# Kernel optimization log

Measured on AMD Instinct MI355X. Metric: run time of the kernel, lower is better.

## Reference

```python
import jax, jax.numpy as jnp
import numpy as np

N_GRAPHS = 256

def gcn_conv(x, src, dst, W, b, n_nodes):
    # PyG GCNConv: add self-loops, symmetric normalization, then aggregate x_j*norm at dst.
    loop = jnp.arange(n_nodes, dtype=src.dtype)
    row = jnp.concatenate([src, loop])
    col = jnp.concatenate([dst, loop])
    h = x @ W  # [N, out]
    deg = jax.ops.segment_sum(jnp.ones_like(col, dtype=h.dtype), col, num_segments=n_nodes)
    dinv = jnp.where(deg > 0, jax.lax.rsqrt(deg), 0.0)
    norm = dinv[row] * dinv[col]  # [E+N]
    msg = h[row] * norm[:, None]
    out = jax.ops.segment_sum(msg, col, num_segments=n_nodes)
    return out + b

def global_mean_pool(x, batch, num_graphs):
    s = jax.ops.segment_sum(x, batch, num_segments=num_graphs)
    cnt = jax.ops.segment_sum(jnp.ones((x.shape[0],), dtype=x.dtype), batch, num_segments=num_graphs)
    return s / jnp.maximum(cnt, 1.0)[:, None]

def setup_inputs() -> dict:
    key = jax.random.key(0)
    ks = jax.random.split(key, 9)
    N, E, F, H = 100000, 3200000, 136, 50
    x = jax.random.normal(ks[0], (N, F), dtype=jnp.float32)
    edge_index = jax.random.randint(ks[1], (2, E), 0, N, dtype=jnp.int64)
    batch = jnp.sort(jax.random.randint(ks[2], (N,), 0, N_GRAPHS, dtype=jnp.int64))
    s1 = 1.0 / np.sqrt(F)
    s2 = 1.0 / np.sqrt(H)
    W1 = jax.random.uniform(ks[3], (F, H), jnp.float32, -s1, s1)
    b1 = jnp.zeros((H,), jnp.float32)
    W2 = jax.random.uniform(ks[4], (H, H), jnp.float32, -s2, s2)
    b2 = jnp.zeros((H,), jnp.float32)
    Wl = jax.random.uniform(ks[5], (H, 1), jnp.float32, -s2, s2)
    bl = jnp.zeros((1,), jnp.float32)
    return {"x": x, "edge_index": edge_index, "batch": batch,
            "W1": W1, "b1": b1, "W2": W2, "b2": b2, "Wl": Wl, "bl": bl}

def reference(x, edge_index, batch, W1, b1, W2, b2, Wl, bl):
    n = x.shape[0]
    src, dst = edge_index[0], edge_index[1]
    h = jax.nn.relu(gcn_conv(x, src, dst, W1, b1, n))
    h = jax.nn.relu(gcn_conv(h, src, dst, W2, b2, n))
    g = global_mean_pool(h, batch, N_GRAPHS)
    # Dropout is inference-identity (deterministic baseline).
    out = jax.nn.sigmoid(g @ Wl + bl)
    return out.flatten()
```

## Files before the change

### kernel.cpp

```cpp
#include <hip/hip_runtime.h>
#include <math.h>

#define HH 50
#define BSH 8
#define BSZ 256
#define CH 8192
#define SCH 4096

typedef float floatx2 __attribute__((ext_vector_type(2)));

__device__ __forceinline__ unsigned int f2bf_pair(float f0, float f1) {
    unsigned int u0 = __float_as_uint(f0);
    unsigned int u1 = __float_as_uint(f1);
    u0 = (u0 + 0x7FFFu + ((u0 >> 16) & 1u)) >> 16;
    u1 = (u1 + 0x7FFFu + ((u1 >> 16) & 1u)) >> 16;
    return u0 | (u1 << 16);
}
__device__ __forceinline__ float bf_lo(unsigned int p) { return __uint_as_float(p << 16); }
__device__ __forceinline__ float bf_hi(unsigned int p) { return __uint_as_float(p & 0xFFFF0000u); }

__device__ __forceinline__ unsigned int pack4_fp8(float f0, float f1, float f2, float f3) {
    int r = 0;
    r = __builtin_amdgcn_cvt_pk_fp8_f32(f0, f1, r, false);
    r = __builtin_amdgcn_cvt_pk_fp8_f32(f2, f3, r, true);
    return (unsigned int)r;
}

__global__ void histA_kernel(const int* __restrict__ ei, int E, int NB, int NC,
                             int* __restrict__ blockHist) {
    __shared__ int hist[512];
    int c = blockIdx.x;
    int tid = threadIdx.x;
    for (int i = tid; i < 512; i += 256) hist[i] = 0;
    __syncthreads();
    int beg = c * CH, end = min(E, beg + CH);
    for (int i = beg + tid; i < end; i += 256) {
        int d = ei[(size_t)E + i];
        atomicAdd(&hist[d >> BSH], 1);
    }
    __syncthreads();
    for (int i = tid; i < NB; i += 256) blockHist[i * NC + c] = hist[i];
}

__global__ void scan1_kernel(const int* __restrict__ bh, int M, int* __restrict__ csum) {
    __shared__ int red[4];
    int tid = threadIdx.x;
    int lane = tid & 63, wv = tid >> 6;
    int base = blockIdx.x * SCH + tid * 16;
    int s = 0;
    if (base + 16 <= M) {
#pragma unroll
        for (int j = 0; j < 4; j++) {
            int4 v = *(const int4*)(bh + base + 4 * j);
            s += v.x + v.y + v.z + v.w;
        }
    } else {
        for (int j = 0; j < 16 && base + j < M; j++) s += bh[base + j];
    }
    for (int off = 1; off < 64; off <<= 1) s += __shfl_xor(s, off);
    if (lane == 0) red[wv] = s;
    __syncthreads();
    if (tid == 0) csum[blockIdx.x] = red[0] + red[1] + red[2] + red[3];
}

__global__ void scan2_kernel(int* __restrict__ csum, int nb,
                             int* __restrict__ rowptr, int N, int E) {
    int lane = threadIdx.x;
    int v = (lane < nb) ? csum[lane] : 0;
    int orig = v;
    for (int off = 1; off < 64; off <<= 1) {
        int u = __shfl_up(v, off);
        if (lane >= off) v += u;
    }
    if (lane < nb) csum[lane] = v - orig;
    if (lane == 0) rowptr[N] = E;
}

__global__ void scan3_kernel(const int* __restrict__ bh, int M, const int* __restrict__ csum,
                             int* __restrict__ scanned) {
    __shared__ int wsum[4];
    int tid = threadIdx.x;
    int lane = tid & 63, wv = tid >> 6;
    int base = blockIdx.x * SCH + tid * 16;
    int a[16];
#pragma unroll
    for (int j = 0; j < 16; j++) a[j] = 0;
    if (base + 16 <= M) {
#pragma unroll
        for (int j = 0; j < 4; j++) {
            int4 v = *(const int4*)(bh + base + 4 * j);
            a[4 * j] = v.x; a[4 * j + 1] = v.y; a[4 * j + 2] = v.z; a[4 * j + 3] = v.w;
        }
    } else {
        for (int j = 0; j < 16 && base + j < M; j++) a[j] = bh[base + j];
    }
    int t = 0;
#pragma unroll
    for (int j = 0; j < 16; j++) t += a[j];
    int inc = t;
    for (int off = 1; off < 64; off <<= 1) {
        int u = __shfl_up(inc, off);
        if (lane >= off) inc += u;
    }
    if (lane == 63) wsum[wv] = inc;
    __syncthreads();
    int wb = 0;
    for (int w = 0; w < wv; w++) wb += wsum[w];
    int run = csum[blockIdx.x] + wb + (inc - t);
    if (base + 16 <= M) {
#pragma unroll
        for (int j = 0; j < 4; j++) {
            int4 o;
            o.x = run; run += a[4 * j];
            o.y = run; run += a[4 * j + 1];
            o.z = run; run += a[4 * j + 2];
            o.w = run; run += a[4 * j + 3];
            *(int4*)(scanned + base + 4 * j) = o;
        }
    } else {
        for (int j = 0; j < 16 && base + j < M; j++) { scanned[base + j] = run; run += a[j]; }
    }
}

__global__ void scatterB_kernel(const int* __restrict__ ei, int E, int NB, int NC,
                                const int* __restrict__ blockHist,
                                const int* __restrict__ scanned, int* __restrict__ ebuf) {
    __shared__ int part[512];
    __shared__ int lofs[512];
    __shared__ int gofs[512];
    __shared__ int cur[512];
    __shared__ int epack[CH];
    int c = blockIdx.x;
    int tid = threadIdx.x;
    int v = (tid < NB) ? blockHist[tid * NC + c] : 0;
    part[tid] = v;
    __syncthreads();
    for (int off = 1; off < 512; off <<= 1) {
        int u = (tid >= off) ? part[tid - off] : 0;
        __syncthreads();
        part[tid] += u;
        __syncthreads();
    }
    int ex = (tid == 0) ? 0 : part[tid - 1];
    lofs[tid] = ex;
    cur[tid] = ex;
    if (tid < NB) gofs[tid] = scanned[tid * NC + c];
    __syncthreads();
    int beg = c * CH, end = min(E, beg + CH), len = end - beg;
    for (int i = beg + tid; i < end; i += 512) {
        int s = ei[i];
        int d = ei[(size_t)E + i];
        int b = d >> BSH;
        int pos = atomicAdd(&cur[b], 1);
        epack[pos] = ((d & (BSZ - 1)) << 17) | s;
    }
    __syncthreads();
    for (int j = tid; j < len; j += 512) {
        int lo = 0, hi = NB - 1;
        while (lo < hi) { int mid = (lo + hi + 1) >> 1; if (lofs[mid] <= j) lo = mid; else hi = mid - 1; }
        ebuf[gofs[lo] + (j - lofs[lo])] = epack[j];
    }
}

__global__ void buildC_kernel(const int* __restrict__ ebuf, const int* __restrict__ scanned,
                              int NB, int NC, int N, int E,
                              int* __restrict__ rowptr, float* __restrict__ dinv,
                              int* __restrict__ colidx) {
    __shared__ int cnt[BSZ], woff[BSZ], part[BSZ];
    int b = blockIdx.x;
    int tid = threadIdx.x;
    int ebeg = scanned[b * NC];
    int eend = (b == NB - 1) ? E : scanned[(b + 1) * NC];
    if (tid < BSZ) cnt[tid] = 0;
    __syncthreads();
    for (int i = ebeg + tid; i < eend; i += 512) {
        atomicAdd(&cnt[ebuf[i] >> 17], 1);
    }
    __syncthreads();
    if (tid < BSZ) part[tid] = cnt[tid];
    __syncthreads();
    for (int off = 1; off < BSZ; off <<= 1) {
        int v = 0;
        if (tid < BSZ && tid >= off) v = part[tid - off];
        __syncthreads();
        if (tid < BSZ) part[tid] += v;
        __syncthreads();
    }
    if (tid < BSZ) {
        int ex = (tid == 0) ? 0 : part[tid - 1];
        woff[tid] = ex;
        int node = (b << BSH) + tid;
        if (node < N) {
            rowptr[node] = ebeg + ex;
            dinv[node] = 1.0f / sqrtf((float)(cnt[tid] + 1));
        }
    }
    __syncthreads();
    for (int i = ebeg + tid; i < eend; i += 512) {
        int p = ebuf[i];
        int dl = p >> 17;
        int s = p & 0x1FFFF;
        int pos = atomicAdd(&woff[dl], 1);
        colidx[ebeg + pos] = s;
    }
}

__global__ void gemm_f32_kernel(const float* __restrict__ in, int K, int f4stride,
                                const float* __restrict__ W, int H,
                                const float* __restrict__ dinv,
                                unsigned int* __restrict__ hsA,
                                unsigned int* __restrict__ hsB, int N) {
    __shared__ float xs[16][128];
    __shared__ float ws[16][64];
    int tid = threadIdx.x;
    int row0 = blockIdx.x * 128;
    int rg = tid >> 3;
    int cg = tid & 7;
    int rl = tid >> 1;
    int h  = tid & 1;
    float acc[4][8];
#pragma unroll
    for (int r = 0; r < 4; r++)
#pragma unroll
        for (int c = 0; c < 8; c++) acc[r][c] = 0.0f;
    const float4* inf4 = (const float4*)in;
    int rowA = row0 + rl;

    for (int k0 = 0; k0 < K; k0 += 16) {
        for (int i = tid; i < 1024; i += 256) {
            int k = i >> 6, c = i & 63;
            ws[k][c] = (k0 + k < K && c < H) ? W[(k0 + k) * H + c] : 0.0f;
        }
        {
            int qa = h, qb = h + 2;
            int g1 = min((k0 >> 2) + qa, f4stride - 1);
            int g2 = min((k0 >> 2) + qb, f4stride - 1);
            float4 xv1 = make_float4(0.f, 0.f, 0.f, 0.f), xv2 = xv1;
            if (rowA < N) {
                xv1 = inf4[(size_t)rowA * f4stride + g1];
                xv2 = inf4[(size_t)rowA * f4stride + g2];
            }
            xs[qa * 4 + 0][rl] = xv1.x; xs[qa * 4 + 1][rl] = xv1.y;
            xs[qa * 4 + 2][rl] = xv1.z; xs[qa * 4 + 3][rl] = xv1.w;
            xs[qb * 4 + 0][rl] = xv2.x; xs[qb * 4 + 1][rl] = xv2.y;
            xs[qb * 4 + 2][rl] = xv2.z; xs[qb * 4 + 3][rl] = xv2.w;
        }
        __syncthreads();
#pragma unroll
        for (int k = 0; k < 16; k++) {
            float4 xa = *(const float4*)&xs[k][rg * 4];
            float4 wa = *(const float4*)&ws[k][cg * 8];
            float4 wb = *(const float4*)&ws[k][cg * 8 + 4];
            float xr[4] = {xa.x, xa.y, xa.z, xa.w};
            float wc[8] = {wa.x, wa.y, wa.z, wa.w, wb.x, wb.y, wb.z, wb.w};
#pragma unroll
            for (int r = 0; r < 4; r++)
#pragma unroll
                for (int c = 0; c < 8; c++) acc[r][c] += xr[r] * wc[c];
        }
        __syncthreads();
    }
#pragma unroll
    for (int r = 0; r < 4; r++) {
        int row = row0 + rg * 4 + r;
        if (row < N) {
            float dv = dinv[row];
            uint2 o;
            o.x = pack4_fp8(acc[r][0] * dv, acc[r][1] * dv, acc[r][2] * dv, acc[r][3] * dv);
            o.y = pack4_fp8(acc[r][4] * dv, acc[r][5] * dv, acc[r][6] * dv, acc[r][7] * dv);
            if (cg < 4) ((uint2*)(hsA + (size_t)row * 8))[cg] = o;
            else        ((uint2*)(hsB + (size_t)row * 8))[cg - 4] = o;
        }
    }
}

__global__ void gemm_bf16_kernel(const unsigned int* __restrict__ in, int K,
                                 const float* __restrict__ W, int H,
                                 const float* __restrict__ dinv,
                                 unsigned int* __restrict__ hsA,
                                 unsigned int* __restrict__ hsB, int N) {
    __shared__ float xs[16][128];
    __shared__ float ws[16][64];
    int tid = threadIdx.x;
    int row0 = blockIdx.x * 128;
    int rg = tid >> 3;
    int cg = tid & 7;
    int rl = tid >> 1;
    int h  = tid & 1;
    float acc[4][8];
#pragma unroll
    for (int r = 0; r < 4; r++)
#pragma unroll
        for (int c = 0; c < 8; c++) acc[r][c] = 0.0f;
    const uint2* inu2 = (const uint2*)in;
    int rowA = row0 + rl;
    int KP = 64;

    for (int k0 = 0; k0 < KP; k0 += 16) {
        for (int i = tid; i < 1024; i += 256) {
            int k = i >> 6, c = i & 63;
            ws[k][c] = (k0 + k < K && c < H) ? W[(k0 + k) * H + c] : 0.0f;
        }
        {
            int qa = h, qb = h + 2;
            int g1 = (k0 >> 2) + qa;
            int g2 = (k0 >> 2) + qb;
            uint2 xv1 = make_uint2(0u, 0u), xv2 = xv1;
            if (rowA < N) {
                xv1 = inu2[(size_t)rowA * 16 + g1];
                xv2 = inu2[(size_t)rowA * 16 + g2];
            }
            xs[qa * 4 + 0][rl] = bf_lo(xv1.x); xs[qa * 4 + 1][rl] = bf_hi(xv1.x);
            xs[qa * 4 + 2][rl] = bf_lo(xv1.y); xs[qa * 4 + 3][rl] = bf_hi(xv1.y);
            xs[qb * 4 + 0][rl] = bf_lo(xv2.x); xs[qb * 4 + 1][rl] = bf_hi(xv2.x);
            xs[qb * 4 + 2][rl] = bf_lo(xv2.y); xs[qb * 4 + 3][rl] = bf_hi(xv2.y);
        }
        __syncthreads();
#pragma unroll
        for (int k = 0; k < 16; k++) {
            float4 xa = *(const float4*)&xs[k][rg * 4];
            float4 wa = *(const float4*)&ws[k][cg * 8];
            float4 wb = *(const float4*)&ws[k][cg * 8 + 4];
            float xr[4] = {xa.x, xa.y, xa.z, xa.w};
            float wc[8] = {wa.x, wa.y, wa.z, wa.w, wb.x, wb.y, wb.z, wb.w};
#pragma unroll
            for (int r = 0; r < 4; r++)
#pragma unroll
                for (int c = 0; c < 8; c++) acc[r][c] += xr[r] * wc[c];
        }
        __syncthreads();
    }
#pragma unroll
    for (int r = 0; r < 4; r++) {
        int row = row0 + rg * 4 + r;
        if (row < N) {
            float dv = dinv[row];
            uint2 o;
            o.x = pack4_fp8(acc[r][0] * dv, acc[r][1] * dv, acc[r][2] * dv, acc[r][3] * dv);
            o.y = pack4_fp8(acc[r][4] * dv, acc[r][5] * dv, acc[r][6] * dv, acc[r][7] * dv);
            if (cg < 4) ((uint2*)(hsA + (size_t)row * 8))[cg] = o;
            else        ((uint2*)(hsB + (size_t)row * 8))[cg - 4] = o;
        }
    }
}

__global__ void agg_half_kernel(const unsigned int* __restrict__ hsh,
                                const int* __restrict__ rowptr, const int* __restrict__ colidx,
                                const float* __restrict__ dinv, const float* __restrict__ bias,
                                int cbase, unsigned int* __restrict__ outbuf, int N) {
    int t = blockIdx.x * blockDim.x + threadIdx.x;
    int node = t >> 3;
    int q = t & 7;
    if (node >= N) return;
    const unsigned int* basq = hsh + q;
    unsigned int sv = basq[(size_t)node * 8];
    floatx2 plo = __builtin_amdgcn_cvt_pk_f32_fp8((int)sv, false);
    floatx2 phi = __builtin_amdgcn_cvt_pk_f32_fp8((int)sv, true);
    float a0 = plo[0], a1 = plo[1], a2 = phi[0], a3 = phi[1];
    int beg = rowptr[node], end = rowptr[node + 1];
    int e = beg;
    for (; e + 4 <= end; e += 4) {
        int s0 = colidx[e], s1 = colidx[e + 1], s2 = colidx[e + 2], s3 = colidx[e + 3];
        unsigned int v0 = basq[(size_t)s0 * 8];
        unsigned int v1 = basq[(size_t)s1 * 8];
        unsigned int v2 = basq[(size_t)s2 * 8];
        unsigned int v3 = basq[(size_t)s3 * 8];
        floatx2 l0 = __builtin_amdgcn_cvt_pk_f32_fp8((int)v0, false);
        floatx2 h0 = __builtin_amdgcn_cvt_pk_f32_fp8((int)v0, true);
        floatx2 l1 = __builtin_amdgcn_cvt_pk_f32_fp8((int)v1, false);
        floatx2 h1 = __builtin_amdgcn_cvt_pk_f32_fp8((int)v1, true);
        floatx2 l2 = __builtin_amdgcn_cvt_pk_f32_fp8((int)v2, false);
        floatx2 h2 = __builtin_amdgcn_cvt_pk_f32_fp8((int)v2, true);
        floatx2 l3 = __builtin_amdgcn_cvt_pk_f32_fp8((int)v3, false);
        floatx2 h3 = __builtin_amdgcn_cvt_pk_f32_fp8((int)v3, true);
        a0 += (l0[0] + l1[0]) + (l2[0] + l3[0]);
        a1 += (l0[1] + l1[1]) + (l2[1] + l3[1]);
        a2 += (h0[0] + h1[0]) + (h2[0] + h3[0]);
        a3 += (h0[1] + h1[1]) + (h2[1] + h3[1]);
    }
    for (; e < end; e++) {
        int s0 = colidx[e];
        unsigned int v0 = basq[(size_t)s0 * 8];
        floatx2 l0 = __builtin_amdgcn_cvt_pk_f32_fp8((int)v0, false);
        floatx2 h0 = __builtin_amdgcn_cvt_pk_f32_fp8((int)v0, true);
        a0 += l0[0]; a1 += l0[1]; a2 += h0[0]; a3 += h0[1];
    }
    float dv = dinv[node];
    int c0 = cbase + q * 4;
    float b0 = (c0 + 0 < HH) ? bias[c0 + 0] : 0.0f;
    float b1 = (c0 + 1 < HH) ? bias[c0 + 1] : 0.0f;
    float b2 = (c0 + 2 < HH) ? bias[c0 + 2] : 0.0f;
    float b3 = (c0 + 3 < HH) ? bias[c0 + 3] : 0.0f;
    float r0 = fmaxf(a0 * dv + b0, 0.0f);
    float r1 = fmaxf(a1 * dv + b1, 0.0f);
    float r2 = fmaxf(a2 * dv + b2, 0.0f);
    float r3 = fmaxf(a3 * dv + b3, 0.0f);
    uint2 w;
    if (c0 >= HH) { w.x = 0u; w.y = 0u; }
    else { w.x = f2bf_pair(r0, r1); w.y = f2bf_pair(r2, r3); }
    ((uint2*)outbuf)[(size_t)node * 16 + (cbase >> 2) + q] = w;
}

__global__ void pool_head_kernel(const unsigned int* __restrict__ h,
                                 const int* __restrict__ batch, int N,
                                 const float* __restrict__ Wl, const float* __restrict__ bl,
                                 float* __restrict__ out, int G) {
    __shared__ float4 red[16][16];
    int b = blockIdx.x;
    int t = threadIdx.x;
    int sub = t >> 4, q = t & 15;
    int beg, end;
    {
        int lo = 0, hi = N;
        while (lo < hi) { int mid = (lo + hi) >> 1; if (batch[mid] < b) lo = mid + 1; else hi = mid; }
        beg = lo;
        lo = 0; hi = N;
        while (lo < hi) { int mid = (lo + hi) >> 1; if (batch[mid] < b + 1) lo = mid + 1; else hi = mid; }
        end = lo;
    }
    const uint2* base = (const uint2*)h;
    float4 acc = make_float4(0.f, 0.f, 0.f, 0.f);
    for (int node = beg + sub; node < end; node += 16) {
        uint2 v = base[(size_t)node * 16 + q];
        acc.x += bf_lo(v.x); acc.y += bf_hi(v.x); acc.z += bf_lo(v.y); acc.w += bf_hi(v.y);
    }
    red[sub][q] = acc;
    __syncthreads();
#pragma unroll
    for (int off = 8; off >= 1; off >>= 1) {
        if (sub < off) {
            float4 a = red[sub][q], c = red[sub + off][q];
            a.x += c.x; a.y += c.y; a.z += c.z; a.w += c.w;
            red[sub][q] = a;
        }
        __syncthreads();
    }
    if (t == 0) {
        const float* g = (const float*)&red[0][0];
        float dot = 0.0f;
        for (int c = 0; c < HH; c++) dot += g[c] * Wl[c];
        float cnt = (float)(end - beg);
        float x = dot / fmaxf(cnt, 1.0f) + bl[0];
        out[b] = 1.0f / (1.0f + expf(-x));
    }
}

extern "C" void kernel_launch(void* const* d_in, const int* in_sizes, int n_in,
                              void* d_out, int out_size, void* d_ws, size_t ws_size,
                              hipStream_t stream) {
    const float* x     = (const float*)d_in[0];
    const int*   ei    = (const int*)d_in[1];
    const int*   batch = (const int*)d_in[2];
    const float* W1    = (const float*)d_in[3];
    const float* b1    = (const float*)d_in[4];
    const float* W2    = (const float*)d_in[5];
    const float* b2    = (const float*)d_in[6];
    const float* Wl    = (const float*)d_in[7];
    const float* bl    = (const float*)d_in[8];
    float* out = (float*)d_out;

    int N = in_sizes[2];
    int E = in_sizes[1] / 2;
    int F = in_sizes[0] / N;
    int G = out_size;

    int NB = (N + BSZ - 1) >> BSH;
    int NC = (E + CH - 1) / CH;
    int M  = NB * NC;
    int NS = (M + SCH - 1) / SCH;

    char* ws = (char*)d_ws;
    size_t off = 0;
    auto alloc = [&](size_t bytes) -> void* {
        void* p = ws + off;
        off += (bytes + 255) & ~(size_t)255;
        return p;
    };
    size_t halfBytes = (size_t)N * 32;
    size_t bufBytes  = (size_t)N * 128;
    size_t ebufBytes = (size_t)E * 4;
    float*        dinv      = (float*)alloc((size_t)N * 4);
    int*          rowptr    = (int*)alloc((size_t)(N + 1) * 4);
    int*          colidx    = (int*)alloc(ebufBytes);
    unsigned int* hsA       = (unsigned int*)alloc(halfBytes);
    unsigned int* hsB       = (unsigned int*)alloc(halfBytes);
    unsigned int* buf       = (unsigned int*)alloc(bufBytes > ebufBytes ? bufBytes : ebufBytes);
    int*          blockHist = (int*)alloc((size_t)M * 4);
    int*          scanned   = (int*)alloc((size_t)M * 4);
    int*          csum      = (int*)alloc((size_t)NS * 4 + 256);
    int*          ebuf      = (int*)buf;

    histA_kernel<<<NC, 256, 0, stream>>>(ei, E, NB, NC, blockHist);
    scan1_kernel<<<NS, 256, 0, stream>>>(blockHist, M, csum);
    scan2_kernel<<<1, 64, 0, stream>>>(csum, NS, rowptr, N, E);
    scan3_kernel<<<NS, 256, 0, stream>>>(blockHist, M, csum, scanned);
    scatterB_kernel<<<NC, 512, 0, stream>>>(ei, E, NB, NC, blockHist, scanned, ebuf);
    buildC_kernel<<<NB, 512, 0, stream>>>(ebuf, scanned, NB, NC, N, E, rowptr, dinv, colidx);

    int aggBlocks = ((N * 8) + 255) / 256;
    int gemmBlocks = (N + 127) / 128;

    gemm_f32_kernel<<<gemmBlocks, 256, 0, stream>>>(x, F, F / 4, W1, HH, dinv, hsA, hsB, N);
    agg_half_kernel<<<aggBlocks, 256, 0, stream>>>(hsA, rowptr, colidx, dinv, b1, 0,  buf, N);
    agg_half_kernel<<<aggBlocks, 256, 0, stream>>>(hsB, rowptr, colidx, dinv, b1, 32, buf, N);

    gemm_bf16_kernel<<<gemmBlocks, 256, 0, stream>>>(buf, 50, W2, HH, dinv, hsA, hsB, N);
    agg_half_kernel<<<aggBlocks, 256, 0, stream>>>(hsA, rowptr, colidx, dinv, b2, 0,  buf, N);
    agg_half_kernel<<<aggBlocks, 256, 0, stream>>>(hsB, rowptr, colidx, dinv, b2, 32, buf, N);

    pool_head_kernel<<<G, 256, 0, stream>>>(buf, batch, N, Wl, bl, out, G);
}
```

Measured before the change: 257.7 us.

## Replace FP32 SIMT GEMMs with bf16 MFMA 16x16x32 kernels

Both dense transforms (x@W1 and h@W2) are rewritten to use bf16 MFMA instructions. Each wave handles 16 rows, the weights are staged transposed in bf16 in LDS, and results go through an LDS tile so the epilogue can scale by dinv and pack to fp8. This targets the FP32 FMA cost and shared-memory traffic of the old tiled GEMMs, at the price of rounding x and W1 to bf16, which adds precision loss. The GEMMs are a small part of a pipeline dominated by aggregation, so the overall effect is bounded.

```diff
diff --git a/kernel.cpp b/kernel.cpp
--- a/kernel.cpp
+++ b/kernel.cpp
@@ -8,6 +8,10 @@
 #define SCH 4096
 
 typedef float floatx2 __attribute__((ext_vector_type(2)));
+typedef float f32x4 __attribute__((ext_vector_type(4)));
+typedef short short8v __attribute__((ext_vector_type(8)));
+
+union ABfrag { short8v s; unsigned int u[4]; };
 
 __device__ __forceinline__ unsigned int f2bf_pair(float f0, float f1) {
     unsigned int u0 = __float_as_uint(f0);
@@ -205,142 +209,130 @@
     }
 }
 
-__global__ void gemm_f32_kernel(const float* __restrict__ in, int K, int f4stride,
-                                const float* __restrict__ W, int H,
-                                const float* __restrict__ dinv,
-                                unsigned int* __restrict__ hsA,
-                                unsigned int* __restrict__ hsB, int N) {
-    __shared__ float xs[16][128];
-    __shared__ float ws[16][64];
-    int tid = threadIdx.x;
-    int row0 = blockIdx.x * 128;
-    int rg = tid >> 3;
-    int cg = tid & 7;
-    int rl = tid >> 1;
-    int h  = tid & 1;
-    float acc[4][8];
-#pragma unroll
-    for (int r = 0; r < 4; r++)
-#pragma unroll
-        for (int c = 0; c < 8; c++) acc[r][c] = 0.0f;
-    const float4* inf4 = (const float4*)in;
-    int rowA = row0 + rl;
-
-    for (int k0 = 0; k0 < K; k0 += 16) {
-        for (int i = tid; i < 1024; i += 256) {
-            int k = i >> 6, c = i & 63;
-            ws[k][c] = (k0 + k < K && c < H) ? W[(k0 + k) * H + c] : 0.0f;
-        }
-        {
-            int qa = h, qb = h + 2;
-            int g1 = min((k0 >> 2) + qa, f4stride - 1);
-            int g2 = min((k0 >> 2) + qb, f4stride - 1);
-            float4 xv1 = make_float4(0.f, 0.f, 0.f, 0.f), xv2 = xv1;
-            if (rowA < N) {
-                xv1 = inf4[(size_t)rowA * f4stride + g1];
-                xv2 = inf4[(size_t)rowA * f4stride + g2];
-            }
-            xs[qa * 4 + 0][rl] = xv1.x; xs[qa * 4 + 1][rl] = xv1.y;
-            xs[qa * 4 + 2][rl] = xv1.z; xs[qa * 4 + 3][rl] = xv1.w;
-            xs[qb * 4 + 0][rl] = xv2.x; xs[qb * 4 + 1][rl] = xv2.y;
-            xs[qb * 4 + 2][rl] = xv2.z; xs[qb * 4 + 3][rl] = xv2.w;
-        }
-        __syncthreads();
-#pragma unroll
-        for (int k = 0; k < 16; k++) {
-            float4 xa = *(const float4*)&xs[k][rg * 4];
-            float4 wa = *(const float4*)&ws[k][cg * 8];
-            float4 wb = *(const float4*)&ws[k][cg * 8 + 4];
-            float xr[4] = {xa.x, xa.y, xa.z, xa.w};
-            float wc[8] = {wa.x, wa.y, wa.z, wa.w, wb.x, wb.y, wb.z, wb.w};
-#pragma unroll
-            for (int r = 0; r < 4; r++)
-#pragma unroll
-                for (int c = 0; c < 8; c++) acc[r][c] += xr[r] * wc[c];
-        }
-        __syncthreads();
-    }
+__global__ void gemm1_mfma(const float* __restrict__ x, int K, int H,
+                           const float* __restrict__ W,
+                           const float* __restrict__ dinv,
+                           unsigned int* __restrict__ hsA,
+                           unsigned int* __restrict__ hsB, int N) {
+    const int KP = 160, S = 168;
+    __shared__ unsigned short wsT[64 * S];
+    __shared__ float ls[4][16][64];
+    int tid = threadIdx.x;
+    int w = tid >> 6, lane = tid & 63;
+    int row0 = blockIdx.x * 64 + w * 16;
+    for (int i = tid; i < KP * 64; i += 256) {
+        int k = i >> 6, col = i & 63;
+        float v = (k < K && col < H) ? W[k * H + col] : 0.0f;
+        wsT[col * S + k] = (unsigned short)(f2bf_pair(v, 0.0f) & 0xFFFFu);
+    }
+    __syncthreads();
+
+    int arow = row0 + (lane & 15);
+    int kgrp = (lane >> 4) * 8;
+    f32x4 acc0 = 0.0f, acc1 = 0.0f, acc2 = 0.0f, acc3 = 0.0f;
+    for (int k0 = 0; k0 < KP; k0 += 32) {
+        int koff = k0 + kgrp;
+        ABfrag a; a.u[0] = 0; a.u[1] = 0; a.u[2] = 0; a.u[3] = 0;
+        if (arow < N && koff < K) {
+            const float* xp = x + (size_t)arow * K + koff;
+            float4 v1 = *(const float4*)xp;
+            float4 v2 = *(const float4*)(xp + 4);
+            a.u[0] = f2bf_pair(v1.x, v1.y); a.u[1] = f2bf_pair(v1.z, v1.w);
+            a.u[2] = f2bf_pair(v2.x, v2.y); a.u[3] = f2bf_pair(v2.z, v2.w);
+        }
+        ABfrag b0, b1, b2, b3;
+        b0.s = *(const short8v*)&wsT[(0 * 16 + (lane & 15)) * S + koff];
+        b1.s = *(const short8v*)&wsT[(1 * 16 + (lane & 15)) * S + koff];
+        b2.s = *(const short8v*)&wsT[(2 * 16 + (lane & 15)) * S + koff];
+        b3.s = *(const short8v*)&wsT[(3 * 16 + (lane & 15)) * S + koff];
+        acc0 = __builtin_amdgcn_mfma_f32_16x16x32_bf16(a.s, b0.s, acc0, 0, 0, 0);
+        acc1 = __builtin_amdgcn_mfma_f32_16x16x32_bf16(a.s, b1.s, acc1, 0, 0, 0);
+        acc2 = __builtin_amdgcn_mfma_f32_16x16x32_bf16(a.s, b2.s, acc2, 0, 0, 0);
+        acc3 = __builtin_amdgcn_mfma_f32_16x16x32_bf16(a.s, b3.s, acc3, 0, 0, 0);
+    }
+    int r4 = (lane >> 4) * 4;
 #pragma unroll
     for (int r = 0; r < 4; r++) {
-        int row = row0 + rg * 4 + r;
-        if (row < N) {
-            float dv = dinv[row];
-            uint2 o;
-            o.x = pack4_fp8(acc[r][0] * dv, acc[r][1] * dv, acc[r][2] * dv, acc[r][3] * dv);
-            o.y = pack4_fp8(acc[r][4] * dv, acc[r][5] * dv, acc[r][6] * dv, acc[r][7] * dv);
-            if (cg < 4) ((uint2*)(hsA + (size_t)row * 8))[cg] = o;
-            else        ((uint2*)(hsB + (size_t)row * 8))[cg - 4] = o;
-        }
-    }
-}
-
-__global__ void gemm_bf16_kernel(const unsigned int* __restrict__ in, int K,
-                                 const float* __restrict__ W, int H,
-                                 const float* __restrict__ dinv,
-                                 unsigned int* __restrict__ hsA,
-                                 unsigned int* __restrict__ hsB, int N) {
-    __shared__ float xs[16][128];
-    __shared__ float ws[16][64];
-    int tid = threadIdx.x;
-    int row0 = blockIdx.x * 128;
-    int rg = tid >> 3;
-    int cg = tid & 7;
-    int rl = tid >> 1;
-    int h  = tid & 1;
-    float acc[4][8];
-#pragma unroll
-    for (int r = 0; r < 4; r++)
-#pragma unroll
-        for (int c = 0; c < 8; c++) acc[r][c] = 0.0f;
-    const uint2* inu2 = (const uint2*)in;
-    int rowA = row0 + rl;
-    int KP = 64;
-
-    for (int k0 = 0; k0 < KP; k0 += 16) {
-        for (int i = tid; i < 1024; i += 256) {
-            int k = i >> 6, c = i & 63;
-            ws[k][c] = (k0 + k < K && c < H) ? W[(k0 + k) * H + c] : 0.0f;
-        }
-        {
-            int qa = h, qb = h + 2;
-            int g1 = (k0 >> 2) + qa;
-            int g2 = (k0 >> 2) + qb;
-            uint2 xv1 = make_uint2(0u, 0u), xv2 = xv1;
-            if (rowA < N) {
-                xv1 = inu2[(size_t)rowA * 16 + g1];
-                xv2 = inu2[(size_t)rowA * 16 + g2];
-            }
-            xs[qa * 4 + 0][rl] = bf_lo(xv1.x); xs[qa * 4 + 1][rl] = bf_hi(xv1.x);
-            xs[qa * 4 + 2][rl] = bf_lo(xv1.y); xs[qa * 4 + 3][rl] = bf_hi(xv1.y);
-            xs[qb * 4 + 0][rl] = bf_lo(xv2.x); xs[qb * 4 + 1][rl] = bf_hi(xv2.x);
-            xs[qb * 4 + 2][rl] = bf_lo(xv2.y); xs[qb * 4 + 3][rl] = bf_hi(xv2.y);
-        }
-        __syncthreads();
-#pragma unroll
-        for (int k = 0; k < 16; k++) {
-            float4 xa = *(const float4*)&xs[k][rg * 4];
-            float4 wa = *(const float4*)&ws[k][cg * 8];
-            float4 wb = *(const float4*)&ws[k][cg * 8 + 4];
-            float xr[4] = {xa.x, xa.y, xa.z, xa.w};
-            float wc[8] = {wa.x, wa.y, wa.z, wa.w, wb.x, wb.y, wb.z, wb.w};
-#pragma unroll
-            for (int r = 0; r < 4; r++)
-#pragma unroll
-                for (int c = 0; c < 8; c++) acc[r][c] += xr[r] * wc[c];
-        }
-        __syncthreads();
-    }
+        ls[w][r4 + r][0 * 16 + (lane & 15)] = acc0[r];
+        ls[w][r4 + r][1 * 16 + (lane & 15)] = acc1[r];
+        ls[w][r4 + r][2 * 16 + (lane & 15)] = acc2[r];
+        ls[w][r4 + r][3 * 16 + (lane & 15)] = acc3[r];
+    }
+    __syncthreads();
+    int prow = lane >> 2, cg = lane & 3;
+    int row = row0 + prow;
+    if (row < N) {
+        float dv = dinv[row];
+        const float* lr = &ls[w][prow][cg * 16];
+        uint4 o;
+        o.x = pack4_fp8(lr[0] * dv, lr[1] * dv, lr[2] * dv, lr[3] * dv);
+        o.y = pack4_fp8(lr[4] * dv, lr[5] * dv, lr[6] * dv, lr[7] * dv);
+        o.z = pack4_fp8(lr[8] * dv, lr[9] * dv, lr[10] * dv, lr[11] * dv);
+        o.w = pack4_fp8(lr[12] * dv, lr[13] * dv, lr[14] * dv, lr[15] * dv);
+        if (cg < 2) ((uint4*)(hsA + (size_t)row * 8))[cg] = o;
+        else        ((uint4*)(hsB + (size_t)row * 8))[cg - 2] = o;
+    }
+}
+
+__global__ void gemm2_mfma(const unsigned int* __restrict__ in, int K, int H,
+                           const float* __restrict__ W,
+                           const float* __restrict__ dinv,
+                           unsigned int* __restrict__ hsA,
+                           unsigned int* __restrict__ hsB, int N) {
+    const int KP = 64, S = 72;
+    __shared__ unsigned short wsT[64 * S];
+    __shared__ float ls[4][16][64];
+    int tid = threadIdx.x;
+    int w = tid >> 6, lane = tid & 63;
+    int row0 = blockIdx.x * 64 + w * 16;
+    for (int i = tid; i < KP * 64; i += 256) {
+        int k = i >> 6, col = i & 63;
+        float v = (k < K && col < H) ? W[k * H + col] : 0.0f;
+        wsT[col * S + k] = (unsigned short)(f2bf_pair(v, 0.0f) & 0xFFFFu);
+    }
+    __syncthreads();
+
+    int arow = row0 + (lane & 15);
+    int kgrp = (lane >> 4) * 8;
+    f32x4 acc0 = 0.0f, acc1 = 0.0f, acc2 = 0.0f, acc3 = 0.0f;
+    for (int k0 = 0; k0 < KP; k0 += 32) {
+        int koff = k0 + kgrp;
+        ABfrag a; a.u[0] = 0; a.u[1] = 0; a.u[2] = 0; a.u[3] = 0;
+        if (arow < N) {
+            uint4 v = *(const uint4*)(in + (size_t)arow * 32 + (koff >> 1));
+            a.u[0] = v.x; a.u[1] = v.y; a.u[2] = v.z; a.u[3] = v.w;
+        }
+        ABfrag b0, b1, b2, b3;
+        b0.s = *(const short8v*)&wsT[(0 * 16 + (lane & 15)) * S + koff];
+        b1.s = *(const short8v*)&wsT[(1 * 16 + (lane & 15)) * S + koff];
+        b2.s = *(const short8v*)&wsT[(2 * 16 + (lane & 15)) * S + koff];
+        b3.s = *(const short8v*)&wsT[(3 * 16 + (lane & 15)) * S + koff];
+        acc0 = __builtin_amdgcn_mfma_f32_16x16x32_bf16(a.s, b0.s, acc0, 0, 0, 0);
+        acc1 = __builtin_amdgcn_mfma_f32_16x16x32_bf16(a.s, b1.s, acc1, 0, 0, 0);
+        acc2 = __builtin_amdgcn_mfma_f32_16x16x32_bf16(a.s, b2.s, acc2, 0, 0, 0);
+        acc3 = __builtin_amdgcn_mfma_f32_16x16x32_bf16(a.s, b3.s, acc3, 0, 0, 0);
+    }
+    int r4 = (lane >> 4) * 4;
 #pragma unroll
     for (int r = 0; r < 4; r++) {
-        int row = row0 + rg * 4 + r;
-        if (row < N) {
-            float dv = dinv[row];
-            uint2 o;
-            o.x = pack4_fp8(acc[r][0] * dv, acc[r][1] * dv, acc[r][2] * dv, acc[r][3] * dv);
-            o.y = pack4_fp8(acc[r][4] * dv, acc[r][5] * dv, acc[r][6] * dv, acc[r][7] * dv);
-            if (cg < 4) ((uint2*)(hsA + (size_t)row * 8))[cg] = o;
-            else        ((uint2*)(hsB + (size_t)row * 8))[cg - 4] = o;
-        }
+        ls[w][r4 + r][0 * 16 + (lane & 15)] = acc0[r];
+        ls[w][r4 + r][1 * 16 + (lane & 15)] = acc1[r];
+        ls[w][r4 + r][2 * 16 + (lane & 15)] = acc2[r];
+        ls[w][r4 + r][3 * 16 + (lane & 15)] = acc3[r];
+    }
+    __syncthreads();
+    int prow = lane >> 2, cg = lane & 3;
+    int row = row0 + prow;
+    if (row < N) {
+        float dv = dinv[row];
+        const float* lr = &ls[w][prow][cg * 16];
+        uint4 o;
+        o.x = pack4_fp8(lr[0] * dv, lr[1] * dv, lr[2] * dv, lr[3] * dv);
+        o.y = pack4_fp8(lr[4] * dv, lr[5] * dv, lr[6] * dv, lr[7] * dv);
+        o.z = pack4_fp8(lr[8] * dv, lr[9] * dv, lr[10] * dv, lr[11] * dv);
+        o.w = pack4_fp8(lr[12] * dv, lr[13] * dv, lr[14] * dv, lr[15] * dv);
+        if (cg < 2) ((uint4*)(hsA + (size_t)row * 8))[cg] = o;
+        else        ((uint4*)(hsB + (size_t)row * 8))[cg - 2] = o;
     }
 }
 
@@ -498,13 +490,13 @@
     buildC_kernel<<<NB, 512, 0, stream>>>(ebuf, scanned, NB, NC, N, E, rowptr, dinv, colidx);
 
     int aggBlocks = ((N * 8) + 255) / 256;
-    int gemmBlocks = (N + 127) / 128;
-
-    gemm_f32_kernel<<<gemmBlocks, 256, 0, stream>>>(x, F, F / 4, W1, HH, dinv, hsA, hsB, N);
+    int mfmaBlocks = (N + 63) / 64;
+
+    gemm1_mfma<<<mfmaBlocks, 256, 0, stream>>>(x, F, HH, W1, dinv, hsA, hsB, N);
     agg_half_kernel<<<aggBlocks, 256, 0, stream>>>(hsA, rowptr, colidx, dinv, b1, 0,  buf, N);
     agg_half_kernel<<<aggBlocks, 256, 0, stream>>>(hsB, rowptr, colidx, dinv, b1, 32, buf, N);
 
-    gemm_bf16_kernel<<<gemmBlocks, 256, 0, stream>>>(buf, 50, W2, HH, dinv, hsA, hsB, N);
+    gemm2_mfma<<<mfmaBlocks, 256, 0, stream>>>(buf, HH, HH, W2, dinv, hsA, hsB, N);
     agg_half_kernel<<<aggBlocks, 256, 0, stream>>>(hsA, rowptr, colidx, dinv, b2, 0,  buf, N);
     agg_half_kernel<<<aggBlocks, 256, 0, stream>>>(hsB, rowptr, colidx, dinv, b2, 32, buf, N);
 
```

Result: faster. 246.4 us (-4.4%).
